# Kernel tuning notes

Hardware: AMD Instinct MI355X
Metric: run time of the kernel (lower is better)

## Reference

```python
import jax, jax.numpy as jnp
import numpy as np

B, T, H = 4, 2048, 1024
DFF = 4 * H
MAX_DEPTH = 4
TARGET_DEPTH = 2.5
BUDGET_WEIGHT = 0.01
ACT_TAU = 0.99


def setup_inputs() -> dict:
    key = jax.random.key(0)
    ks = jax.random.split(key, 6)
    s = 0.02
    return {
        "x": jax.random.normal(ks[0], (B, T, H), dtype=jnp.float32),
        "Wb1": jax.random.normal(ks[1], (H, DFF), dtype=jnp.float32) * s,
        "bb1": jnp.zeros((DFF,), dtype=jnp.float32),
        "Wb2": jax.random.normal(ks[2], (DFF, H), dtype=jnp.float32) * s,
        "bb2": jnp.zeros((H,), dtype=jnp.float32),
        "Rw1": jax.random.normal(ks[3], (MAX_DEPTH - 1, H + 1, H // 2), dtype=jnp.float32) * s,
        "Rb1": jnp.zeros((MAX_DEPTH - 1, H // 2), dtype=jnp.float32),
        "Rw2": jax.random.normal(ks[4], (MAX_DEPTH - 1, H // 2, 1), dtype=jnp.float32) * s,
        "Rb2": jnp.zeros((MAX_DEPTH - 1, 1), dtype=jnp.float32),
    }


def _body(x, Wb1, bb1, Wb2, bb2):
    # transformer-style FFN body, exact (erf) GELU to match torch nn.GELU
    h = jax.nn.gelu(jnp.einsum("btd,df->btf", x, Wb1) + bb1, approximate=False)
    return jnp.einsum("btf,fd->btd", h, Wb2) + bb2


def reference(x, Wb1, bb1, Wb2, bb2, Rw1, Rb1, Rw2, Rb2):
    # mandatory first pass
    x = _body(x, Wb1, bb1, Wb2, bb2)
    lead = x.shape[:-1]  # (B, T)
    weight_sum = jnp.ones(lead, dtype=x.dtype)
    cumulative_p = jnp.zeros(lead, dtype=x.dtype)
    still_running = jnp.ones(lead, dtype=x.dtype)
    for i in range(MAX_DEPTH - 1):
        # router: concat spike-rate feature (zeros: no scalar aux from body)
        feat = jnp.concatenate([x, jnp.zeros(lead + (1,), dtype=x.dtype)], axis=-1)
        h = jax.nn.gelu(jnp.einsum("btf,fm->btm", feat, Rw1[i]) + Rb1[i], approximate=False)
        logit = (jnp.einsum("btm,mo->bto", h, Rw2[i]) + Rb2[i])[..., 0]
        p = jax.nn.sigmoid(logit)
        # ACT remainder trick
        remainder = jnp.clip(1.0 - cumulative_p, 0.0)
        would_halt = cumulative_p + p >= ACT_TAU
        weight = jnp.where(would_halt, remainder, p) * still_running
        # soft depth mix
        x_new = _body(x, Wb1, bb1, Wb2, bb2)
        w = weight[..., None]
        x = w * x_new + (1.0 - w) * x
        weight_sum = weight_sum + weight
        cumulative_p = cumulative_p + weight
        still_running = still_running * (~would_halt).astype(x.dtype)
    avg_depth = weight_sum.mean()
    budget_loss = BUDGET_WEIGHT * jnp.square(jax.nn.relu(avg_depth - TARGET_DEPTH))
    return x, budget_loss
```

## Files before the change

kernel.cpp:

```cpp
#include <hip/hip_runtime.h>
#include <hip/hip_bf16.h>
#include <math.h>

typedef __bf16 bf16_t;
typedef __attribute__((ext_vector_type(8))) __bf16 bf16x8;
typedef __attribute__((ext_vector_type(4))) __bf16 bf16x4;
typedef __attribute__((ext_vector_type(4))) float f32x4;

#define NTOK 8192
#define HDIM 1024
#define DFF  4096
#define RHID 512

__device__ __forceinline__ float gelu_exact(float v) {
  return 0.5f * v * (1.0f + erff(v * 0.70710678118654752f));
}

__device__ __forceinline__ float gelu_fast(float v) {
  const float g = 1.5957691216057308f * (v + 0.044715f * v * v * v);
  return v / (1.0f + __expf(-g));
}

__device__ __forceinline__ void async_cp16(void* lds, const void* g) {
  __builtin_amdgcn_global_load_lds(
      (__attribute__((address_space(1))) void*)g,
      (__attribute__((address_space(3))) void*)lds, 16, 0, 0);
}

__device__ __forceinline__ void remap_tile(int g, int& mt, int& nt) {
  mt = ((g & 7) << 3) | ((g >> 3) & 7);
  nt = g >> 6;
}

template<int MODE, bool WRITE_OUT, int WM, int WN, bool COMPACT>
__device__ __forceinline__ void body_tile(
    int mt, int nt,
    const bf16_t* __restrict__ A, const bf16_t* __restrict__ Bt,
    const float* __restrict__ bias, int N, int K,
    bf16_t* __restrict__ Hout, float* __restrict__ Xout,
    bf16_t* __restrict__ Xb, bf16_t* __restrict__ Xlo,
    const float* __restrict__ Wmix,
    const int* __restrict__ idxl, int cnt,
    bf16_t* As, bf16_t* Bs)
{
  constexpr int BM  = WM * 32;
  constexpr int BN  = WN * 32;
  constexpr int ACH = BM / 32;
  constexpr int BCH = BN / 32;
  const int tid  = threadIdx.x;
  const int lane = tid & 63;
  const int wv   = tid >> 6;
  const int wm   = wv >> 1;
  const int wn   = wv & 1;
  const int lr   = lane & 15;
  const int quad = lane >> 4;
  const int m0 = mt * BM;
  const int n0 = nt * BN;

  f32x4 acc[WM][WN];
#pragma unroll
  for (int i = 0; i < WM; ++i)
#pragma unroll
    for (int j = 0; j < WN; ++j)
      acc[i][j] = (f32x4){0.f, 0.f, 0.f, 0.f};

  const int c   = tid;
  const int row = c >> 3;
  const int ks  = (((c & 7) - (row & 7)) & 7) * 8;
  size_t aoff[ACH];
#pragma unroll
  for (int t = 0; t < ACH; ++t) {
    int rr = m0 + row + 32 * t;
    if (COMPACT && MODE == 0) rr = idxl[rr < cnt ? rr : cnt - 1];
    aoff[t] = (size_t)rr * K + ks;
  }
  const bf16_t* Bgb = Bt + (size_t)(n0 + row) * K + ks;
  char* lAb = (char*)As + c * 16;
  char* lBb = (char*)Bs + c * 16;

  for (int kb = 0; kb < K; kb += 64) {
    __syncthreads();
#pragma unroll
    for (int t = 0; t < ACH; ++t)
      async_cp16(lAb + 4096 * t, A + aoff[t] + kb);
#pragma unroll
    for (int t = 0; t < BCH; ++t)
      async_cp16(lBb + 4096 * t, Bgb + (size_t)32 * t * K + kb);
    __syncthreads();
#pragma unroll
    for (int kk = 0; kk < 2; ++kk) {
      const int kg = kk * 4 + quad;
      bf16x8 af[WM], bfr[WN];
#pragma unroll
      for (int i = 0; i < WM; ++i) {
        const int ra = wm * (WM * 16) + i * 16 + lr;
        af[i] = *(const bf16x8*)&As[ra * 64 + ((kg + ra) & 7) * 8];
      }
#pragma unroll
      for (int j = 0; j < WN; ++j) {
        const int rb = wn * (WN * 16) + j * 16 + lr;
        bfr[j] = *(const bf16x8*)&Bs[rb * 64 + ((kg + rb) & 7) * 8];
      }
#pragma unroll
      for (int i = 0; i < WM; ++i)
#pragma unroll
        for (int j = 0; j < WN; ++j)
          acc[i][j] = __builtin_amdgcn_mfma_f32_16x16x32_bf16(af[i], bfr[j], acc[i][j], 0, 0, 0);
    }
  }

#pragma unroll
  for (int i = 0; i < WM; ++i) {
#pragma unroll
    for (int r = 0; r < 4; ++r) {
      const int gm = m0 + wm * (WM * 16) + i * 16 + quad * 4 + r;
      bool act_row = true;
      int tok = gm;
      if (COMPACT && MODE == 2) {
        act_row = gm < cnt;
        tok = idxl[act_row ? gm : cnt - 1];
      }
      float wmix = 0.f, onemw = 0.f;
      if (MODE == 2) { wmix = Wmix[tok]; onemw = 1.f - wmix; }
#pragma unroll
      for (int j = 0; j < WN; ++j) {
        const int gn = n0 + wn * (WN * 16) + j * 16 + lr;
        float v = acc[i][j][r] + bias[gn];
        if (MODE == 0) {
          Hout[(size_t)gm * N + gn] = (bf16_t)gelu_fast(v);
        } else {
          const size_t idx = (size_t)tok * N + gn;
          if (MODE == 2) {
            const float xold = (float)Xb[idx] + (float)Xlo[idx];
            v = wmix * v + onemw * xold;
          }
          if (act_row) {
            const bf16_t hi = (bf16_t)v;
            Xb[idx]  = hi;
            Xlo[idx] = (bf16_t)(v - (float)hi);
            if (WRITE_OUT) Xout[idx] = v;
          }
        }
      }
    }
  }
}

template<bool COMPACT>
__device__ __forceinline__ void router_tile(
    int mt, int nt,
    const bf16_t* __restrict__ Ah, const bf16_t* __restrict__ Al,
    const bf16_t* __restrict__ Bh, const bf16_t* __restrict__ Bl,
    const float* __restrict__ bias, float* __restrict__ Hr,
    const int* __restrict__ idxl, int cnt,
    bf16_t* Ahs, bf16_t* Als, bf16_t* Bhs, bf16_t* Bls)
{
  const int K = HDIM, N = RHID;
  const int tid  = threadIdx.x;
  const int lane = tid & 63;
  const int wv   = tid >> 6;
  const int wm   = wv >> 1;
  const int wn   = wv & 1;
  const int lr   = lane & 15;
  const int quad = lane >> 4;
  const int m0 = mt * 128;
  const int n0 = nt * 128;

  f32x4 acc[4][4];
#pragma unroll
  for (int i = 0; i < 4; ++i)
#pragma unroll
    for (int j = 0; j < 4; ++j)
      acc[i][j] = (f32x4){0.f, 0.f, 0.f, 0.f};

  const int c0 = tid;
  const int c1 = tid + 256;
  const int r0 = c0 >> 2, r1 = c1 >> 2;
  const int ks0 = ((c0 ^ r0) & 3) * 8;
  const int ks1 = ((c1 ^ r1) & 3) * 8;
  int tr0 = m0 + r0, tr1 = m0 + r1;
  if (COMPACT) {
    tr0 = idxl[tr0 < cnt ? tr0 : cnt - 1];
    tr1 = idxl[tr1 < cnt ? tr1 : cnt - 1];
  }
  const size_t aoff0 = (size_t)tr0 * K + ks0;
  const size_t aoff1 = (size_t)tr1 * K + ks1;
  const size_t boff0 = (size_t)(n0 + r0) * K + ks0;
  const size_t boff1 = (size_t)(n0 + r1) * K + ks1;
  const int sw = ((quad ^ lr) & 3) * 8;

  for (int k0 = 0; k0 < K; k0 += 32) {
    __syncthreads();
    async_cp16((char*)Ahs + c0 * 16, Ah + aoff0 + k0);
    async_cp16((char*)Ahs + c1 * 16, Ah + aoff1 + k0);
    async_cp16((char*)Als + c0 * 16, Al + aoff0 + k0);
    async_cp16((char*)Als + c1 * 16, Al + aoff1 + k0);
    async_cp16((char*)Bhs + c0 * 16, Bh + boff0 + k0);
    async_cp16((char*)Bhs + c1 * 16, Bh + boff1 + k0);
    async_cp16((char*)Bls + c0 * 16, Bl + boff0 + k0);
    async_cp16((char*)Bls + c1 * 16, Bl + boff1 + k0);
    __syncthreads();
    bf16x8 ah[4], al[4], bh[4], bl[4];
#pragma unroll
    for (int i = 0; i < 4; ++i) {
      const int ao = (wm * 64 + i * 16 + lr) * 32 + sw;
      ah[i] = *(const bf16x8*)&Ahs[ao];
      al[i] = *(const bf16x8*)&Als[ao];
    }
#pragma unroll
    for (int j = 0; j < 4; ++j) {
      const int bo = (wn * 64 + j * 16 + lr) * 32 + sw;
      bh[j] = *(const bf16x8*)&Bhs[bo];
      bl[j] = *(const bf16x8*)&Bls[bo];
    }
#pragma unroll
    for (int i = 0; i < 4; ++i)
#pragma unroll
      for (int j = 0; j < 4; ++j) {
        acc[i][j] = __builtin_amdgcn_mfma_f32_16x16x32_bf16(ah[i], bh[j], acc[i][j], 0, 0, 0);
        acc[i][j] = __builtin_amdgcn_mfma_f32_16x16x32_bf16(al[i], bh[j], acc[i][j], 0, 0, 0);
        acc[i][j] = __builtin_amdgcn_mfma_f32_16x16x32_bf16(ah[i], bl[j], acc[i][j], 0, 0, 0);
      }
  }

#pragma unroll
  for (int i = 0; i < 4; ++i)
#pragma unroll
    for (int r = 0; r < 4; ++r) {
      const int gm = m0 + wm * 64 + i * 16 + quad * 4 + r;
      bool act_row = true;
      int tok = gm;
      if (COMPACT) {
        act_row = gm < cnt;
        tok = idxl[act_row ? gm : cnt - 1];
      }
#pragma unroll
      for (int j = 0; j < 4; ++j) {
        const int gn = n0 + wn * 64 + j * 16 + lr;
        if (act_row) Hr[(size_t)tok * N + gn] = gelu_exact(acc[i][j][r] + bias[gn]);
      }
    }
}

template<int MODE, bool WRITE_OUT, bool COMPACT>
__global__ __launch_bounds__(256, 4)
void k_gemm(const bf16_t* __restrict__ A, const bf16_t* __restrict__ Bt,
            const float* __restrict__ bias, int N, int K,
            float* __restrict__ Xout, bf16_t* __restrict__ Xb,
            bf16_t* __restrict__ Xlo, const float* __restrict__ Wmix,
            const int* __restrict__ idxl, const int* __restrict__ cntp)
{
  __shared__ __align__(16) bf16_t sm[16384];
  int cnt = NTOK;
  if (COMPACT) cnt = *cntp;
  int mt, nt;
  remap_tile(blockIdx.x, mt, nt);
  if (COMPACT && mt * 128 >= cnt) return;
  body_tile<MODE, WRITE_OUT, 4, 4, COMPACT>(mt, nt, A, Bt, bias, N, K,
                                            nullptr, Xout, Xb, Xlo, Wmix,
                                            idxl, cnt, sm, sm + 8192);
}

template<bool COMPACT>
__global__ __launch_bounds__(256, 4)
void k_body0_router(const bf16_t* __restrict__ xb, const bf16_t* __restrict__ W1t,
                    const float* __restrict__ bb1, bf16_t* __restrict__ hbuf,
                    const bf16_t* __restrict__ xlo,
                    const bf16_t* __restrict__ R1h, const bf16_t* __restrict__ R1l,
                    const float* __restrict__ Rb1, float* __restrict__ hr,
                    const int* __restrict__ idxl, const int* __restrict__ cntp,
                    int nbody)
{
  __shared__ __align__(16) bf16_t sm[16384];
  int cnt = NTOK;
  if (COMPACT) cnt = *cntp;
  const int g = blockIdx.x;
  if (g < nbody) {
    int mt, nt;
    remap_tile(g, mt, nt);
    if (COMPACT && mt * 128 >= cnt) return;
    body_tile<0, false, 4, 4, COMPACT>(mt, nt, xb, W1t, bb1, DFF, HDIM, hbuf,
                                       nullptr, nullptr, nullptr, nullptr,
                                       idxl, cnt, sm, sm + 8192);
  } else {
    int mt, nt;
    remap_tile(g - nbody, mt, nt);
    if (COMPACT && mt * 128 >= cnt) return;
    router_tile<COMPACT>(mt, nt, xb, xlo, R1h, R1l, Rb1, hr, idxl, cnt,
                         sm, sm + 4096, sm + 8192, sm + 12288);
  }
}

__global__ void act_kernel(const float* __restrict__ Hr,
                           const float* __restrict__ rw2, const float* __restrict__ rb2,
                           float* __restrict__ cum_p, float* __restrict__ still_r,
                           float* __restrict__ wsum, float* __restrict__ wvec,
                           int build, int* __restrict__ cntp, int* __restrict__ idxl)
{
  const int t = blockIdx.x * 4 + (threadIdx.x >> 6);
  const int lane = threadIdx.x & 63;
  float s = 0.f;
#pragma unroll
  for (int j = 0; j < 8; ++j) {
    const int m = lane + j * 64;
    s += Hr[(size_t)t * RHID + m] * rw2[m];
  }
  for (int off = 32; off > 0; off >>= 1) s += __shfl_down(s, off, 64);
  if (lane == 0) {
    const float logit = s + rb2[0];
    const float p = 1.f / (1.f + expf(-logit));
    const float cum = cum_p[t];
    const float still = still_r[t];
    const float rem = fmaxf(1.f - cum, 0.f);
    const bool halt = (cum + p) >= 0.99f;
    const float w = (halt ? rem : p) * still;
    wvec[t] = w;
    wsum[t] += w;
    cum_p[t] = cum + w;
    if (halt) still_r[t] = 0.f;
    if (build && still > 0.f && !halt) {
      const int pos = atomicAdd(cntp, 1);
      idxl[pos] = t;
    }
  }
}

__global__ void copyout_kernel(const bf16_t* __restrict__ Xb,
                               const bf16_t* __restrict__ Xlo,
                               const float* __restrict__ still,
                               float* __restrict__ Xout)
{
  const int e = blockIdx.x * 256 + threadIdx.x;
  const int t = e >> 8;
  if (still[t] != 0.f) return;
  const bf16x4 hi = ((const bf16x4*)Xb)[e];
  const bf16x4 lo = ((const bf16x4*)Xlo)[e];
  float4 o;
  o.x = (float)hi[0] + (float)lo[0];
  o.y = (float)hi[1] + (float)lo[1];
  o.z = (float)hi[2] + (float)lo[2];
  o.w = (float)hi[3] + (float)lo[3];
  ((float4*)Xout)[e] = o;
}

__device__ __forceinline__ void transpose_tile(
    const float* __restrict__ src, int srcld, int dstld,
    bf16_t* __restrict__ dst, bf16_t* __restrict__ dlo,
    int bx, int by, float* tile )
{
  const int tx = threadIdx.x & 31;
  const int ty = threadIdx.x >> 5;
#pragma unroll
  for (int l = 0; l < 4; ++l)
    tile[(ty + l * 8) * 33 + tx] = src[(size_t)(by * 32 + ty + l * 8) * srcld + bx * 32 + tx];
  __syncthreads();
#pragma unroll
  for (int l = 0; l < 4; ++l) {
    const int c = bx * 32 + ty + l * 8;
    const int r = by * 32 + tx;
    const float v = tile[tx * 33 + ty + l * 8];
    const bf16_t hi = (bf16_t)v;
    dst[(size_t)c * dstld + r] = hi;
    if (dlo) dlo[(size_t)c * dstld + r] = (bf16_t)(v - (float)hi);
  }
}

__global__ void prep_kernel(const float* __restrict__ x,
                            const float* __restrict__ Wb1,
                            const float* __restrict__ Wb2,
                            const float* __restrict__ Rw1,
                            bf16_t* __restrict__ xb,
                            bf16_t* __restrict__ W1t, bf16_t* __restrict__ W2t,
                            bf16_t* __restrict__ R1h, bf16_t* __restrict__ R1l,
                            float* __restrict__ cum0, float* __restrict__ stil0,
                            float* __restrict__ wsum0, int* __restrict__ cntp)
{
  __shared__ float tile[32 * 33];
  const int g = blockIdx.x;
  if (g < 4096) {
    transpose_tile(Wb1, DFF, HDIM, W1t, nullptr, g & 127, g >> 7, tile);
  } else if (g < 8192) {
    const int g2 = g - 4096;
    transpose_tile(Wb2, HDIM, DFF, W2t, nullptr, g2 & 31, g2 >> 5, tile);
  } else if (g < 9728) {
    const int g3 = g - 8192;
    const int i  = g3 >> 9;
    const int r  = g3 & 511;
    transpose_tile(Rw1 + (size_t)i * 1025 * RHID, RHID, HDIM,
                   R1h + (size_t)i * RHID * HDIM, R1l + (size_t)i * RHID * HDIM,
                   r & 15, r >> 4, tile);
  } else if (g < 17920) {
    const int i = (g - 9728) * 256 + threadIdx.x;
    const float4 v = ((const float4*)x)[i];
    bf16x4 hb;
    hb[0] = (bf16_t)v.x; hb[1] = (bf16_t)v.y; hb[2] = (bf16_t)v.z; hb[3] = (bf16_t)v.w;
    ((bf16x4*)xb)[i] = hb;
  } else {
    const int t = (g - 17920) * 256 + threadIdx.x;
    cum0[t] = 0.f; stil0[t] = 1.f; wsum0[t] = 1.f;
    if (t == 0) *cntp = 0;
  }
}

__global__ void finalize_kernel(const float* __restrict__ wsum, float* __restrict__ out)
{
  __shared__ float red[256];
  float s = 0.f;
  for (int i = threadIdx.x; i < NTOK; i += 256) s += wsum[i];
  red[threadIdx.x] = s;
  __syncthreads();
  for (int o = 128; o > 0; o >>= 1) {
    if (threadIdx.x < o) red[threadIdx.x] += red[threadIdx.x + o];
    __syncthreads();
  }
  if (threadIdx.x == 0) {
    const float avg = red[0] / (float)NTOK;
    float d = avg - 2.5f;
    d = fmaxf(d, 0.f);
    out[0] = 0.01f * d * d;
  }
}

extern "C" void kernel_launch(void* const* d_in, const int* in_sizes, int n_in,
                              void* d_out, int out_size, void* d_ws, size_t ws_size,
                              hipStream_t stream) {
  const float* x   = (const float*)d_in[0];
  const float* Wb1 = (const float*)d_in[1];
  const float* bb1 = (const float*)d_in[2];
  const float* Wb2 = (const float*)d_in[3];
  const float* bb2 = (const float*)d_in[4];
  const float* Rw1 = (const float*)d_in[5];
  const float* Rb1 = (const float*)d_in[6];
  const float* Rw2 = (const float*)d_in[7];
  const float* Rb2 = (const float*)d_in[8];
  float* out = (float*)d_out;

  char* ws = (char*)d_ws;
  size_t off = 0;
  auto carve = [&](size_t bytes) -> void* {
    void* p = ws + off;
    off += (bytes + 255) & ~(size_t)255;
    return p;
  };
  bf16_t* xb   = (bf16_t*)carve((size_t)NTOK * HDIM * 2);
  bf16_t* xlo  = (bf16_t*)carve((size_t)NTOK * HDIM * 2);
  bf16_t* hbuf = (bf16_t*)carve((size_t)NTOK * DFF * 2);
  bf16_t* W1t  = (bf16_t*)carve((size_t)HDIM * DFF * 2);
  bf16_t* W2t  = (bf16_t*)carve((size_t)HDIM * DFF * 2);
  bf16_t* R1h  = (bf16_t*)carve((size_t)3 * RHID * HDIM * 2);
  bf16_t* R1l  = (bf16_t*)carve((size_t)3 * RHID * HDIM * 2);
  float*  hr   = (float*)carve((size_t)NTOK * RHID * 4);
  float*  cum  = (float*)carve((size_t)NTOK * 4);
  float*  stil = (float*)carve((size_t)NTOK * 4);
  float*  wsum = (float*)carve((size_t)NTOK * 4);
  float*  wvec = (float*)carve((size_t)NTOK * 4);
  int*    idxl = (int*)carve((size_t)NTOK * 4);
  int*    cntp = (int*)carve(256);

  prep_kernel<<<17952, 256, 0, stream>>>(x, Wb1, Wb2, Rw1, xb, W1t, W2t,
                                         R1h, R1l, cum, stil, wsum, cntp);

  k_body0_router<false><<<2048, 256, 0, stream>>>(
      xb, W1t, bb1, hbuf, xlo, nullptr, nullptr, nullptr, nullptr,
      idxl, cntp, 2048);
  k_gemm<1, false, false><<<512, 256, 0, stream>>>(
      hbuf, W2t, bb2, HDIM, DFF, nullptr, xb, xlo, nullptr, idxl, cntp);

  k_body0_router<false><<<2048 + 256, 256, 0, stream>>>(
      xb, W1t, bb1, hbuf, xlo,
      R1h, R1l, Rb1, hr, idxl, cntp, 2048);
  act_kernel<<<2048, 256, 0, stream>>>(hr, Rw2, Rb2, cum, stil, wsum, wvec,
                                       0, cntp, idxl);
  k_gemm<2, false, false><<<512, 256, 0, stream>>>(
      hbuf, W2t, bb2, HDIM, DFF, nullptr, xb, xlo, wvec, idxl, cntp);

  k_body0_router<false><<<2048 + 256, 256, 0, stream>>>(
      xb, W1t, bb1, hbuf, xlo,
      R1h + (size_t)RHID * HDIM, R1l + (size_t)RHID * HDIM,
      Rb1 + RHID, hr, idxl, cntp, 2048);
  act_kernel<<<2048, 256, 0, stream>>>(hr, Rw2 + RHID, Rb2 + 1,
                                       cum, stil, wsum, wvec, 1, cntp, idxl);
  k_gemm<2, false, false><<<512, 256, 0, stream>>>(
      hbuf, W2t, bb2, HDIM, DFF, nullptr, xb, xlo, wvec, idxl, cntp);

  copyout_kernel<<<8192, 256, 0, stream>>>(xb, xlo, stil, out);

  k_body0_router<true><<<2048 + 256, 256, 0, stream>>>(
      xb, W1t, bb1, hbuf, xlo,
      R1h + (size_t)2 * RHID * HDIM, R1l + (size_t)2 * RHID * HDIM,
      Rb1 + 2 * RHID, hr, idxl, cntp, 2048);
  act_kernel<<<2048, 256, 0, stream>>>(hr, Rw2 + 2 * RHID, Rb2 + 2,
                                       cum, stil, wsum, wvec, 0, cntp, idxl);
  k_gemm<2, true, true><<<512, 256, 0, stream>>>(
      hbuf, W2t, bb2, HDIM, DFF, out, xb, xlo, wvec, idxl, cntp);

  finalize_kernel<<<1, 256, 0, stream>>>(wsum, out + (size_t)NTOK * HDIM);
  (void)in_sizes; (void)n_in; (void)out_size; (void)ws_size;
}
```

Baseline: 1.014 ms.

## Order-preserving compaction, dense tile mapping for compacted grids, fuse halted-row copyout

The atomic-based active-token list built inside act_kernel is replaced by a single-block ballot/prefix-scan compaction kernel that keeps token order deterministic. The separate copyout kernel is folded into the epilogue of the preceding mixing GEMM, which writes fp32 output for halted rows. In compacted launches, tiles are mapped densely (mt = g % mtA) so blocks beyond the active row count exit early rather than depending on the swizzled remap. A-tile offsets are also turned into precomputed pointers. Together these remove a full elementwise pass and tighten the active-token tile layout, at the cost of an extra serial one-block kernel.

Result: faster. 846.2 us (median of 2 runs) (-16.5%).

```diff
diff --git a/kernel.cpp b/kernel.cpp
--- a/kernel.cpp
+++ b/kernel.cpp
@@ -32,14 +32,14 @@
   nt = g >> 6;
 }
 
-template<int MODE, bool WRITE_OUT, int WM, int WN, bool COMPACT>
+template<int MODE, bool WRITE_OUT, bool HALTW, int WM, int WN, bool COMPACT>
 __device__ __forceinline__ void body_tile(
     int mt, int nt,
     const bf16_t* __restrict__ A, const bf16_t* __restrict__ Bt,
     const float* __restrict__ bias, int N, int K,
     bf16_t* __restrict__ Hout, float* __restrict__ Xout,
     bf16_t* __restrict__ Xb, bf16_t* __restrict__ Xlo,
-    const float* __restrict__ Wmix,
+    const float* __restrict__ Wmix, const float* __restrict__ Stil,
     const int* __restrict__ idxl, int cnt,
     bf16_t* As, bf16_t* Bs)
 {
@@ -67,12 +67,12 @@
   const int c   = tid;
   const int row = c >> 3;
   const int ks  = (((c & 7) - (row & 7)) & 7) * 8;
-  size_t aoff[ACH];
+  const bf16_t* Ag[ACH];
 #pragma unroll
   for (int t = 0; t < ACH; ++t) {
     int rr = m0 + row + 32 * t;
     if (COMPACT && MODE == 0) rr = idxl[rr < cnt ? rr : cnt - 1];
-    aoff[t] = (size_t)rr * K + ks;
+    Ag[t] = A + (size_t)rr * K + ks;
   }
   const bf16_t* Bgb = Bt + (size_t)(n0 + row) * K + ks;
   char* lAb = (char*)As + c * 16;
@@ -82,7 +82,7 @@
     __syncthreads();
 #pragma unroll
     for (int t = 0; t < ACH; ++t)
-      async_cp16(lAb + 4096 * t, A + aoff[t] + kb);
+      async_cp16(lAb + 4096 * t, Ag[t] + kb);
 #pragma unroll
     for (int t = 0; t < BCH; ++t)
       async_cp16(lBb + 4096 * t, Bgb + (size_t)32 * t * K + kb);
@@ -120,8 +120,11 @@
         act_row = gm < cnt;
         tok = idxl[act_row ? gm : cnt - 1];
       }
-      float wmix = 0.f, onemw = 0.f;
-      if (MODE == 2) { wmix = Wmix[tok]; onemw = 1.f - wmix; }
+      float wmix = 0.f, onemw = 0.f, st = 1.f;
+      if (MODE == 2) {
+        wmix = Wmix[tok]; onemw = 1.f - wmix;
+        if (HALTW) st = Stil[tok];
+      }
 #pragma unroll
       for (int j = 0; j < WN; ++j) {
         const int gn = n0 + wn * (WN * 16) + j * 16 + lr;
@@ -136,9 +139,11 @@
           }
           if (act_row) {
             const bf16_t hi = (bf16_t)v;
+            const bf16_t lo = (bf16_t)(v - (float)hi);
             Xb[idx]  = hi;
-            Xlo[idx] = (bf16_t)(v - (float)hi);
+            Xlo[idx] = lo;
             if (WRITE_OUT) Xout[idx] = v;
+            if (HALTW && st == 0.f) Xout[idx] = (float)hi + (float)lo;
           }
         }
       }
@@ -242,23 +247,30 @@
     }
 }
 
-template<int MODE, bool WRITE_OUT, bool COMPACT>
+template<int MODE, bool WRITE_OUT, bool HALTW, bool COMPACT>
 __global__ __launch_bounds__(256, 4)
 void k_gemm(const bf16_t* __restrict__ A, const bf16_t* __restrict__ Bt,
             const float* __restrict__ bias, int N, int K,
             float* __restrict__ Xout, bf16_t* __restrict__ Xb,
             bf16_t* __restrict__ Xlo, const float* __restrict__ Wmix,
+            const float* __restrict__ Stil,
             const int* __restrict__ idxl, const int* __restrict__ cntp)
 {
   __shared__ __align__(16) bf16_t sm[16384];
   int cnt = NTOK;
-  if (COMPACT) cnt = *cntp;
   int mt, nt;
-  remap_tile(blockIdx.x, mt, nt);
-  if (COMPACT && mt * 128 >= cnt) return;
-  body_tile<MODE, WRITE_OUT, 4, 4, COMPACT>(mt, nt, A, Bt, bias, N, K,
-                                            nullptr, Xout, Xb, Xlo, Wmix,
-                                            idxl, cnt, sm, sm + 8192);
+  if (COMPACT) {
+    cnt = *cntp;
+    const int mtA = (cnt + 127) >> 7;
+    if ((int)blockIdx.x >= mtA * (N >> 7)) return;
+    mt = blockIdx.x % mtA;
+    nt = blockIdx.x / mtA;
+  } else {
+    remap_tile(blockIdx.x, mt, nt);
+  }
+  body_tile<MODE, WRITE_OUT, HALTW, 4, 4, COMPACT>(
+      mt, nt, A, Bt, bias, N, K, nullptr, Xout, Xb, Xlo, Wmix, Stil,
+      idxl, cnt, sm, sm + 8192);
 }
 
 template<bool COMPACT>
@@ -273,19 +285,35 @@
 {
   __shared__ __align__(16) bf16_t sm[16384];
   int cnt = NTOK;
-  if (COMPACT) cnt = *cntp;
+  int mtA = NTOK >> 7;
+  if (COMPACT) {
+    cnt = *cntp;
+    mtA = (cnt + 127) >> 7;
+  }
   const int g = blockIdx.x;
   if (g < nbody) {
     int mt, nt;
-    remap_tile(g, mt, nt);
-    if (COMPACT && mt * 128 >= cnt) return;
-    body_tile<0, false, 4, 4, COMPACT>(mt, nt, xb, W1t, bb1, DFF, HDIM, hbuf,
-                                       nullptr, nullptr, nullptr, nullptr,
-                                       idxl, cnt, sm, sm + 8192);
+    if (COMPACT) {
+      if (g >= mtA * (DFF >> 7)) return;
+      mt = g % mtA;
+      nt = g / mtA;
+    } else {
+      remap_tile(g, mt, nt);
+    }
+    body_tile<0, false, false, 4, 4, COMPACT>(
+        mt, nt, xb, W1t, bb1, DFF, HDIM, hbuf,
+        nullptr, nullptr, nullptr, nullptr, nullptr,
+        idxl, cnt, sm, sm + 8192);
   } else {
+    const int g2 = g - nbody;
     int mt, nt;
-    remap_tile(g - nbody, mt, nt);
-    if (COMPACT && mt * 128 >= cnt) return;
+    if (COMPACT) {
+      if (g2 >= mtA * (RHID >> 7)) return;
+      mt = g2 % mtA;
+      nt = g2 / mtA;
+    } else {
+      remap_tile(g2, mt, nt);
+    }
     router_tile<COMPACT>(mt, nt, xb, xlo, R1h, R1l, Rb1, hr, idxl, cnt,
                          sm, sm + 4096, sm + 8192, sm + 12288);
   }
@@ -294,8 +322,7 @@
 __global__ void act_kernel(const float* __restrict__ Hr,
                            const float* __restrict__ rw2, const float* __restrict__ rb2,
                            float* __restrict__ cum_p, float* __restrict__ still_r,
-                           float* __restrict__ wsum, float* __restrict__ wvec,
-                           int build, int* __restrict__ cntp, int* __restrict__ idxl)
+                           float* __restrict__ wsum, float* __restrict__ wvec)
 {
   const int t = blockIdx.x * 4 + (threadIdx.x >> 6);
   const int lane = threadIdx.x & 63;
@@ -318,29 +345,35 @@
     wsum[t] += w;
     cum_p[t] = cum + w;
     if (halt) still_r[t] = 0.f;
-    if (build && still > 0.f && !halt) {
-      const int pos = atomicAdd(cntp, 1);
-      idxl[pos] = t;
-    }
-  }
-}
-
-__global__ void copyout_kernel(const bf16_t* __restrict__ Xb,
-                               const bf16_t* __restrict__ Xlo,
-                               const float* __restrict__ still,
-                               float* __restrict__ Xout)
-{
-  const int e = blockIdx.x * 256 + threadIdx.x;
-  const int t = e >> 8;
-  if (still[t] != 0.f) return;
-  const bf16x4 hi = ((const bf16x4*)Xb)[e];
-  const bf16x4 lo = ((const bf16x4*)Xlo)[e];
-  float4 o;
-  o.x = (float)hi[0] + (float)lo[0];
-  o.y = (float)hi[1] + (float)lo[1];
-  o.z = (float)hi[2] + (float)lo[2];
-  o.w = (float)hi[3] + (float)lo[3];
-  ((float4*)Xout)[e] = o;
+  }
+}
+
+__global__ void compact_kernel(const float* __restrict__ still,
+                               int* __restrict__ idxl, int* __restrict__ cntp)
+{
+  __shared__ int wsumS[16];
+  const int tid  = threadIdx.x;
+  const int w    = tid >> 6;
+  const int lane = tid & 63;
+  int base = 0;
+  for (int c = 0; c < 8; ++c) {
+    const int t = c * 1024 + tid;
+    const bool f = still[t] > 0.f;
+    const unsigned long long m = __ballot(f);
+    if (lane == 0) wsumS[w] = __popcll(m);
+    __syncthreads();
+    int woff = 0, tot = 0;
+#pragma unroll
+    for (int i = 0; i < 16; ++i) {
+      const int v = wsumS[i];
+      if (i < w) woff += v;
+      tot += v;
+    }
+    if (f) idxl[base + woff + __popcll(m & ((1ull << lane) - 1ull))] = t;
+    base += tot;
+    __syncthreads();
+  }
+  if (tid == 0) *cntp = base;
 }
 
 __device__ __forceinline__ void transpose_tile(
@@ -463,36 +496,35 @@
   k_body0_router<false><<<2048, 256, 0, stream>>>(
       xb, W1t, bb1, hbuf, xlo, nullptr, nullptr, nullptr, nullptr,
       idxl, cntp, 2048);
-  k_gemm<1, false, false><<<512, 256, 0, stream>>>(
-      hbuf, W2t, bb2, HDIM, DFF, nullptr, xb, xlo, nullptr, idxl, cntp);
+  k_gemm<1, false, false, false><<<512, 256, 0, stream>>>(
+      hbuf, W2t, bb2, HDIM, DFF, nullptr, xb, xlo, nullptr, nullptr,
+      idxl, cntp);
 
   k_body0_router<false><<<2048 + 256, 256, 0, stream>>>(
-      xb, W1t, bb1, hbuf, xlo,
-      R1h, R1l, Rb1, hr, idxl, cntp, 2048);
-  act_kernel<<<2048, 256, 0, stream>>>(hr, Rw2, Rb2, cum, stil, wsum, wvec,
-                                       0, cntp, idxl);
-  k_gemm<2, false, false><<<512, 256, 0, stream>>>(
-      hbuf, W2t, bb2, HDIM, DFF, nullptr, xb, xlo, wvec, idxl, cntp);
+      xb, W1t, bb1, hbuf, xlo, R1h, R1l, Rb1, hr, idxl, cntp, 2048);
+  act_kernel<<<2048, 256, 0, stream>>>(hr, Rw2, Rb2, cum, stil, wsum, wvec);
+  k_gemm<2, false, false, false><<<512, 256, 0, stream>>>(
+      hbuf, W2t, bb2, HDIM, DFF, nullptr, xb, xlo, wvec, nullptr,
+      idxl, cntp);
 
   k_body0_router<false><<<2048 + 256, 256, 0, stream>>>(
       xb, W1t, bb1, hbuf, xlo,
       R1h + (size_t)RHID * HDIM, R1l + (size_t)RHID * HDIM,
       Rb1 + RHID, hr, idxl, cntp, 2048);
   act_kernel<<<2048, 256, 0, stream>>>(hr, Rw2 + RHID, Rb2 + 1,
-                                       cum, stil, wsum, wvec, 1, cntp, idxl);
-  k_gemm<2, false, false><<<512, 256, 0, stream>>>(
-      hbuf, W2t, bb2, HDIM, DFF, nullptr, xb, xlo, wvec, idxl, cntp);
-
-  copyout_kernel<<<8192, 256, 0, stream>>>(xb, xlo, stil, out);
+                                       cum, stil, wsum, wvec);
+  compact_kernel<<<1, 1024, 0, stream>>>(stil, idxl, cntp);
+  k_gemm<2, false, true, false><<<512, 256, 0, stream>>>(
+      hbuf, W2t, bb2, HDIM, DFF, out, xb, xlo, wvec, stil, idxl, cntp);
 
   k_body0_router<true><<<2048 + 256, 256, 0, stream>>>(
       xb, W1t, bb1, hbuf, xlo,
       R1h + (size_t)2 * RHID * HDIM, R1l + (size_t)2 * RHID * HDIM,
       Rb1 + 2 * RHID, hr, idxl, cntp, 2048);
   act_kernel<<<2048, 256, 0, stream>>>(hr, Rw2 + 2 * RHID, Rb2 + 2,
-                                       cum, stil, wsum, wvec, 0, cntp, idxl);
-  k_gemm<2, true, true><<<512, 256, 0, stream>>>(
-      hbuf, W2t, bb2, HDIM, DFF, out, xb, xlo, wvec, idxl, cntp);
+                                       cum, stil, wsum, wvec);
+  k_gemm<2, true, false, true><<<512, 256, 0, stream>>>(
+      hbuf, W2t, bb2, HDIM, DFF, out, xb, xlo, wvec, nullptr, idxl, cntp);
 
   finalize_kernel<<<1, 256, 0, stream>>>(wsum, out + (size_t)NTOK * HDIM);
   (void)in_sizes; (void)n_in; (void)out_size; (void)ws_size;
```
